# Performance work log

Measured on AMD Instinct MI355X. Metric: run time of the kernel, lower is better.

Reference implementation:

```python
import jax, jax.numpy as jnp
import numpy as np

B, L, E, H, T = 8, 4096, 512, 8, 2
D = E // H


def setup_inputs() -> dict:
    key = jax.random.key(0)
    ks = jax.random.split(key, 11)
    s = 0.02
    return {
        "query": jax.random.normal(ks[0], (B, L, E), jnp.float32),
        "key": jax.random.normal(ks[1], (B, L, E), jnp.float32),
        "value": jax.random.normal(ks[2], (B, L, E), jnp.float32),
        "Wq": jax.random.normal(ks[3], (T, E, E), jnp.float32) * s,
        "bq": jax.random.normal(ks[4], (T, E), jnp.float32) * s,
        "Wk": jax.random.normal(ks[5], (T, E, E), jnp.float32) * s,
        "bk": jax.random.normal(ks[6], (T, E), jnp.float32) * s,
        "Wv": jax.random.normal(ks[7], (E, E), jnp.float32) * s,
        "bv": jax.random.normal(ks[8], (E,), jnp.float32) * s,
        "Wout": jax.random.normal(ks[9], (E, E), jnp.float32) * s,
        "bout": jax.random.normal(ks[10], (E,), jnp.float32) * s,
    }


def reference(query, key, value, Wq, bq, Wk, bk, Wv, bv, Wout, bout):
    bsz, tgt_len, embed_dim = query.shape
    src_len = key.shape[1]
    n_head = H
    head_dim = embed_dim // n_head

    # value projection: (B,S,H,D)
    v = (value @ Wv.T + bv).reshape(bsz, src_len, n_head, head_dim)
    # faithful to torch: value.view(-1, bsz*n_head, head_dim).transpose(0,1)
    # WITHOUT permuting to (S,B,H,D) first -> pure memory reinterpretation
    v = jnp.swapaxes(v.reshape(src_len, bsz * n_head, head_dim), 0, 1)  # (BH,S,D)

    # per-term q/k projections -> (T,L,B,H,D) / (T,S,B,H,D)
    q = jnp.einsum('ble,tfe->tblf', query, Wq) + bq[:, None, None, :]
    k = jnp.einsum('bse,tfe->tbsf', key, Wk) + bk[:, None, None, :]
    q = q.reshape(T, bsz, tgt_len, n_head, head_dim).transpose(0, 2, 1, 3, 4)
    k = k.reshape(T, bsz, src_len, n_head, head_dim).transpose(0, 2, 1, 3, 4)

    # act_fun == softmax: q softmax over feature dim, k softmax over sequence dim (dim 0)
    q = jax.nn.softmax(q, axis=-1)
    k = jax.nn.softmax(k, axis=1)

    # flatten: (T, L, B*H, D) -> (T, B*H, L, D)
    q = jnp.swapaxes(q.reshape(T, tgt_len, bsz * n_head, head_dim), 1, 2)
    k = jnp.swapaxes(k.reshape(T, src_len, bsz * n_head, head_dim), 1, 2)

    # cosine positional reweighting (cosFormer): doubles feature dim
    m = max(src_len, tgt_len)
    idx = (np.pi / 2) * jnp.arange(1, m + 1, dtype=q.dtype) / m  # (m,)
    sin_q = jnp.sin(idx[:tgt_len])[None, None, :, None]
    cos_q = jnp.cos(idx[:tgt_len])[None, None, :, None]
    sin_k = jnp.sin(idx[:src_len])[None, None, :, None]
    cos_k = jnp.cos(idx[:src_len])[None, None, :, None]
    q = jnp.concatenate([q * sin_q, q * cos_q], axis=-1)  # (T,BH,L,2D)
    k = jnp.concatenate([k * sin_k, k * cos_k], axis=-1)  # (T,BH,S,2D)

    # linear attention: kv state then output, summed over terms
    kv = jnp.einsum('tnsd,nsm->tndm', k, v)          # (T,BH,2D,D)
    out = jnp.einsum('tnld,tndm->nlm', q, kv)        # (BH,L,D) summed over T

    # back to (B,L,E)
    out = jnp.swapaxes(out, 0, 1).reshape(tgt_len, bsz, embed_dim)
    out = jnp.swapaxes(out, 0, 1)
    return out @ Wout.T + bout
```

## Files before the change

### kernel.cpp

```cpp
#include <hip/hip_runtime.h>
#include <cstdio>

#define E_DIM 512
#define L_DIM 4096
#define B_DIM 8
#define H_DIM 8
#define T_DIM 2
#define M_ROWS 32768

typedef __attribute__((ext_vector_type(8))) __bf16 bf16x8;
typedef __attribute__((ext_vector_type(4))) float f32x4;

static __device__ __forceinline__ unsigned short f2bf(float f) {
  unsigned int u = __float_as_uint(f);
  return (unsigned short)((u + 0x7FFFu + ((u >> 16) & 1u)) >> 16);
}
static __device__ __forceinline__ unsigned int pkbf(float lo, float hi) {
  return (unsigned int)f2bf(lo) | ((unsigned int)f2bf(hi) << 16);
}
static __device__ __forceinline__ float bf2f(unsigned short u) {
  return __uint_as_float((unsigned int)u << 16);
}
static __device__ __forceinline__ void unpk8(uint4 u, float* f) {
  f[0] = bf2f((unsigned short)u.x); f[1] = bf2f((unsigned short)(u.x >> 16));
  f[2] = bf2f((unsigned short)u.y); f[3] = bf2f((unsigned short)(u.y >> 16));
  f[4] = bf2f((unsigned short)u.z); f[5] = bf2f((unsigned short)(u.z >> 16));
  f[6] = bf2f((unsigned short)u.w); f[7] = bf2f((unsigned short)(u.w >> 16));
}
static __device__ __forceinline__ int swz64(int row, int e) {
  return row * 64 + ((((e >> 3) ^ row) & 7) << 3) + (e & 7);
}
static __device__ __forceinline__ int swz128(int row, int e) {
  return row * 128 + ((((e >> 3) ^ row) & 7) << 3) + ((e >> 3) & 8) * 8 + (e & 7);
}
static __device__ __forceinline__ void gl_lds16(const unsigned short* g,
                                                unsigned short* l) {
  __builtin_amdgcn_global_load_lds(
      (const __attribute__((address_space(1))) unsigned int*)g,
      (__attribute__((address_space(3))) unsigned int*)l, 16, 0, 0);
}

__global__ void prep_kernel(const float* __restrict__ Wq, const float* __restrict__ Wk,
                            const float* __restrict__ Wv, const float* __restrict__ Wout,
                            unsigned short* __restrict__ wbf,
                            float* __restrict__ sintab, float* __restrict__ costab) {
  int blk = blockIdx.x;
  if (blk < 768) {
    int i8 = blk * 256 + threadIdx.x;
    const float* src;
    if (i8 < 65536) src = Wq + (size_t)i8 * 8;
    else if (i8 < 131072) src = Wk + (size_t)(i8 - 65536) * 8;
    else if (i8 < 163840) src = Wv + (size_t)(i8 - 131072) * 8;
    else src = Wout + (size_t)(i8 - 163840) * 8;
    float4 a = *(const float4*)src;
    float4 b = *(const float4*)(src + 4);
    uint4 o;
    o.x = pkbf(a.x, a.y); o.y = pkbf(a.z, a.w);
    o.z = pkbf(b.x, b.y); o.w = pkbf(b.z, b.w);
    *(uint4*)(wbf + (size_t)i8 * 8) = o;
  } else {
    int i = (blk - 768) * 256 + threadIdx.x;
    float idx = 1.57079632679489662f * (float)(i + 1) / (float)L_DIM;
    sintab[i] = sinf(idx);
    costab[i] = cosf(idx);
  }
}

__global__ void convf2b(const float* __restrict__ src, unsigned short* __restrict__ dst,
                        int n8) {
  for (int i = blockIdx.x * blockDim.x + threadIdx.x; i < n8; i += gridDim.x * blockDim.x) {
    float4 a = *(const float4*)(src + (size_t)i * 8);
    float4 b = *(const float4*)(src + (size_t)i * 8 + 4);
    uint4 o;
    o.x = pkbf(a.x, a.y); o.y = pkbf(a.z, a.w);
    o.z = pkbf(b.x, b.y); o.w = pkbf(b.z, b.w);
    *(uint4*)(dst + (size_t)i * 8) = o;
  }
}

#define YHALF 16777216
template <int MODE, int NBL2>
__global__ __launch_bounds__(256, 2) void gemm_xwt(
    const unsigned short* __restrict__ X, const unsigned short* __restrict__ W,
    const float* __restrict__ bias, void* __restrict__ Yv,
    float* __restrict__ psum) {
  __shared__ __align__(16) unsigned short smem[32768];
  __shared__ float sf2[256];
  const int tid = threadIdx.x;
  const int id = blockIdx.x;
  const int j = id >> 3;
  const int mb = (id & 7) * 32 + (j >> NBL2);
  const int nb = j & ((1 << NBL2) - 1);
  const int m0 = mb * 128, n0 = nb * 128;
  const int lane = tid & 63;
  const int w = tid >> 6;
  const int wr = w >> 1, wc = w & 1;
  const int lr = lane & 15;
  const int lk = (lane >> 4) * 8;
  const int rq = lane >> 4;
  const int srow = lane >> 3;
  const int gsrc8 = ((lane & 7) ^ srow) * 8;
  f32x4 acc[4][4];
#pragma unroll
  for (int i = 0; i < 4; ++i)
#pragma unroll
    for (int jj = 0; jj < 4; ++jj) acc[i][jj] = (f32x4){0.f, 0.f, 0.f, 0.f};

#pragma unroll
  for (int i = 0; i < 4; ++i) {
    int rb = w * 32 + i * 8;
    gl_lds16(X + (size_t)(m0 + rb + srow) * 512 + gsrc8, &smem[rb * 64]);
    gl_lds16(W + (size_t)(n0 + rb + srow) * 512 + gsrc8, &smem[8192 + rb * 64]);
  }
  __syncthreads();

#pragma unroll
  for (int step = 0; step < 8; ++step) {
    const int cur = step & 1;
    if (step < 7) {
      unsigned short* Ab = smem + (cur ^ 1) * 16384;
      const int kn = (step + 1) * 64;
#pragma unroll
      for (int i = 0; i < 4; ++i) {
        int rb = w * 32 + i * 8;
        gl_lds16(X + (size_t)(m0 + rb + srow) * 512 + kn + gsrc8, &Ab[rb * 64]);
        gl_lds16(W + (size_t)(n0 + rb + srow) * 512 + kn + gsrc8,
                 &Ab[8192 + rb * 64]);
      }
    }
    const unsigned short* As = smem + cur * 16384;
    const unsigned short* Bs = As + 8192;
#pragma unroll
    for (int kk = 0; kk < 2; ++kk) {
      bf16x8 av[4], bv[4];
      int ke = kk * 32 + lk;
#pragma unroll
      for (int fm = 0; fm < 4; ++fm)
        av[fm] = *(const bf16x8*)&As[swz64(wr * 64 + fm * 16 + lr, ke)];
#pragma unroll
      for (int fn = 0; fn < 4; ++fn)
        bv[fn] = *(const bf16x8*)&Bs[swz64(wc * 64 + fn * 16 + lr, ke)];
#pragma unroll
      for (int fm = 0; fm < 4; ++fm)
#pragma unroll
        for (int fn = 0; fn < 4; ++fn)
          acc[fm][fn] = __builtin_amdgcn_mfma_f32_16x16x32_bf16(av[fm], bv[fn],
                                                                acc[fm][fn], 0, 0, 0);
    }
    __syncthreads();
  }

  if (MODE == 0 || MODE == 2) {
    unsigned short* Cs = smem;
    if (MODE == 0) {
#pragma unroll
      for (int fn = 0; fn < 4; ++fn) {
        int col = wc * 64 + fn * 16 + lr;
        float bb = bias[n0 + col];
#pragma unroll
        for (int fm = 0; fm < 4; ++fm) {
          int row = wr * 64 + fm * 16 + rq * 4;
#pragma unroll
          for (int jj = 0; jj < 4; ++jj)
            Cs[(row + jj) * 136 + col] = f2bf(acc[fm][fn][jj] + bb);
        }
      }
    } else {
#pragma unroll
      for (int fn = 0; fn < 4; ++fn) {
        int col = wc * 64 + fn * 16 + lr;
        float bb = bias[n0 + col];
        float S = 0.f;
#pragma unroll
        for (int fm = 0; fm < 4; ++fm) {
          int row = wr * 64 + fm * 16 + rq * 4;
#pragma unroll
          for (int jj = 0; jj < 4; ++jj) {
            float u = __expf(acc[fm][fn][jj] + bb);
            S += u;
            Cs[(row + jj) * 136 + col] = f2bf(u);
          }
        }
        S += __shfl_xor(S, 16);
        S += __shfl_xor(S, 32);
        if (rq == 0) sf2[wr * 128 + col] = S;
      }
    }
    __syncthreads();
    if (MODE == 2 && tid < 128) {
      float S = sf2[tid] + sf2[128 + tid];
      psum[(size_t)(m0 >> 7) * (128 << NBL2) + n0 + tid] = S;
    }
    unsigned short* Yb = (unsigned short*)Yv + (size_t)(n0 >> 9) * YHALF;
    const int nc = n0 & 511;
#pragma unroll
    for (int i = 0; i < 8; ++i) {
      int idx = tid + i * 256;
      int row = idx >> 4, g = idx & 15;
      *(uint4*)(Yb + (size_t)(m0 + row) * 512 + nc + g * 8) =
          *(const uint4*)&Cs[row * 136 + g * 8];
    }
  } else {
    float* Cf = (float*)smem;
    float* Yf = (float*)Yv;
#pragma unroll
    for (int p = 0; p < 2; ++p) {
      if (p) __syncthreads();
      if (wr == p) {
#pragma unroll
        for (int fn = 0; fn < 4; ++fn) {
          int col = wc * 64 + fn * 16 + lr;
          float bb = bias[n0 + col];
#pragma unroll
          for (int fm = 0; fm < 4; ++fm) {
            int lrow = fm * 16 + rq * 4;
#pragma unroll
            for (int jj = 0; jj < 4; ++jj)
              Cf[(lrow + jj) * 132 + col] = acc[fm][fn][jj] + bb;
          }
        }
      }
      __syncthreads();
#pragma unroll
      for (int i = 0; i < 8; ++i) {
        int idx = tid + i * 256;
        int row = idx >> 5, g = idx & 31;
        *(float4*)(Yf + (size_t)(m0 + p * 64 + row) * 512 + n0 + g * 4) =
            *(const float4*)&Cf[row * 132 + g * 4];
      }
    }
  }
}

__global__ void colsum_reduce2(const float* __restrict__ psum,
                               float* __restrict__ colinv) {
  int t = blockIdx.x >> 4;
  int i = (blockIdx.x & 15) * 256 + threadIdx.x;
  int b = i >> 9, f = i & 511;
  float S = 0.f;
#pragma unroll
  for (int c = 0; c < 32; ++c)
    S += psum[(size_t)(b * 32 + c) * 1024 + t * 512 + f];
  colinv[t * 4096 + i] = 1.f / S;
}

__global__ __launch_bounds__(256) void kv_mfma(
    const unsigned short* __restrict__ Up, const unsigned short* __restrict__ Vpb,
    const float* __restrict__ sintab, const float* __restrict__ costab,
    float* __restrict__ kvpart) {
  __shared__ __align__(16) unsigned short kT[64 * 64];
  __shared__ __align__(16) unsigned short vT[128 * 64];
  const int tid = threadIdx.x;
  const int chunk = blockIdx.x;
  const int n = blockIdx.y;
  const int b = n >> 3, h = n & 7;
  const int lane = tid & 63;
  const int w = tid >> 6;
  const int lr = lane & 15;
  const int lk = (lane >> 4) * 8;
  const int sp = tid & 31;
  const int g = tid >> 5;
  f32x4 acc[4][2];
#pragma unroll
  for (int i = 0; i < 4; ++i) {
    acc[i][0] = (f32x4){0.f, 0.f, 0.f, 0.f};
    acc[i][1] = (f32x4){0.f, 0.f, 0.f, 0.f};
  }

  for (int st = 0; st < 8; ++st) {
    int sA = chunk * 512 + st * 64 + 2 * sp;
    const unsigned short* kp = Up + ((size_t)b * L_DIM + sA) * 512 + h * 64 + g * 8;
    uint4 ka = *(const uint4*)kp;
    uint4 kb = *(const uint4*)(kp + 512);
    int vr = ((sA >> 9) << 12) + ((sA & 511) << 3) + b;
    const unsigned short* vp = Vpb + (size_t)vr * 512 + h * 64 + g * 8;
    uint4 v0 = *(const uint4*)vp;
    uint4 v1 = *(const uint4*)(vp + 8 * 512);
    unsigned short ua[8], ub[8];
    *(uint4*)ua = ka;
    *(uint4*)ub = kb;
    float vA[8], vB[8];
    unpk8(v0, vA);
    unpk8(v1, vB);
    float sS = sintab[sA], sC = costab[sA];
    float tS = sintab[sA + 1], tC = costab[sA + 1];
    __syncthreads();
#pragma unroll
    for (int i = 0; i < 8; ++i) {
      int d = g * 8 + i;
      *(unsigned int*)&kT[swz64(d, 2 * sp)] =
          (unsigned int)ua[i] | ((unsigned int)ub[i] << 16);
    }
#pragma unroll
    for (int i = 0; i < 8; ++i) {
      int m = g * 8 + i;
      *(unsigned int*)&vT[swz64(m, 2 * sp)] = pkbf(vA[i] * sS, vB[i] * tS);
      *(unsigned int*)&vT[swz64(64 + m, 2 * sp)] = pkbf(vA[i] * sC, vB[i] * tC);
    }
    __syncthreads();
#pragma unroll
    for (int kk = 0; kk < 2; ++kk) {
      int ke = kk * 32 + lk;
      bf16x8 av[4], bv[2];
#pragma unroll
      for (int fm = 0; fm < 4; ++fm)
        av[fm] = *(const bf16x8*)&kT[swz64(fm * 16 + lr, ke)];
#pragma unroll
      for (int fn = 0; fn < 2; ++fn)
        bv[fn] = *(const bf16x8*)&vT[swz64(w * 32 + fn * 16 + lr, ke)];
#pragma unroll
      for (int fm = 0; fm < 4; ++fm)
#pragma unroll
        for (int fn = 0; fn < 2; ++fn)
          acc[fm][fn] = __builtin_amdgcn_mfma_f32_16x16x32_bf16(av[fm], bv[fn],
                                                                acc[fm][fn], 0, 0, 0);
    }
  }
  const int rq = lane >> 4;
#pragma unroll
  for (int fn = 0; fn < 2; ++fn) {
    int ncol = w * 32 + fn * 16 + lr;
    int m = ncol & 63;
    int ddbase = (ncol >> 6) * 64;
#pragma unroll
    for (int fm = 0; fm < 4; ++fm) {
#pragma unroll
      for (int jj = 0; jj < 4; ++jj) {
        int dd = ddbase + fm * 16 + rq * 4 + jj;
        kvpart[(((size_t)chunk * 64 + n) * 64 + m) * 128 + dd] = acc[fm][fn][jj];
      }
    }
  }
}

__global__ void kv_reduce_swz(const float* __restrict__ part,
                              const float* __restrict__ colinv,
                              unsigned short* __restrict__ kvT) {
  int i = blockIdx.x * 256 + threadIdx.x;
  float s = 0.f;
#pragma unroll
  for (int c = 0; c < 8; ++c) s += part[(size_t)c * 524288 + i];
  int dd = i & 127;
  int m = (i >> 7) & 63;
  int n = i >> 13;
  float sc = colinv[(n >> 3) * 512 + (n & 7) * 64 + (dd & 63)];
  int gg = dd >> 3;
  int e = ((gg & 8) | ((gg ^ m) & 7)) * 8 + (dd & 7);
  kvT[(size_t)(i >> 7) * 128 + e] = f2bf(s * sc);
}

__global__ __launch_bounds__(256) void out_fused(
    const unsigned short* __restrict__ Qp0, const unsigned short* __restrict__ Qp1,
    const unsigned short* __restrict__ kvT,
    const float* __restrict__ sintab, const float* __restrict__ costab,
    unsigned short* __restrict__ Yb) {
  __shared__ __align__(16) unsigned short q2s[64 * 128];
  __shared__ __align__(16) unsigned short kvs[2][64 * 128];
  const int tid = threadIdx.x;
  const int lc = blockIdx.x;
  const int n = blockIdx.y;
  const int b = n >> 3, h = n & 7;
  const int lane = tid & 63;
  const int w = tid >> 6;
  {
    const uint4* s0 = (const uint4*)(kvT + (size_t)n * 8192);
    const uint4* s1 = (const uint4*)(kvT + 524288 + (size_t)n * 8192);
    uint4* d0 = (uint4*)kvs[0];
    uint4* d1 = (uint4*)kvs[1];
#pragma unroll
    for (int i = 0; i < 4; ++i) {
      d0[tid + i * 256] = s0[tid + i * 256];
      d1[tid + i * 256] = s1[tid + i * 256];
    }
  }
  const int l0 = lc * 64;
  const int wr = w >> 1, wc = w & 1;
  const int lr = lane & 15;
  const int lk = (lane >> 4) * 8;
  const int rq = lane >> 4;
  f32x4 acc[2][2];
  acc[0][0] = acc[0][1] = acc[1][0] = acc[1][1] = (f32x4){0.f, 0.f, 0.f, 0.f};
#pragma unroll
  for (int t = 0; t < 2; ++t) {
    const unsigned short* Qp = t ? Qp1 : Qp0;
    if (t) __syncthreads();
#pragma unroll
    for (int i = 0; i < 2; ++i) {
      int idx = tid + i * 256;
      int row = idx >> 3;
      int g = idx & 7;
      uint4 q = *(const uint4*)(Qp + ((size_t)b * L_DIM + l0 + row) * 512 +
                                h * 64 + g * 8);
      float v[8];
      unpk8(q, v);
      float m8 = fmaxf(fmaxf(fmaxf(v[0], v[1]), fmaxf(v[2], v[3])),
                       fmaxf(fmaxf(v[4], v[5]), fmaxf(v[6], v[7])));
      m8 = fmaxf(m8, __shfl_xor(m8, 1));
      m8 = fmaxf(m8, __shfl_xor(m8, 2));
      m8 = fmaxf(m8, __shfl_xor(m8, 4));
      float e[8], s8;
#pragma unroll
      for (int k = 0; k < 8; ++k) e[k] = __expf(v[k] - m8);
      s8 = ((e[0] + e[1]) + (e[2] + e[3])) + ((e[4] + e[5]) + (e[6] + e[7]));
      s8 += __shfl_xor(s8, 1);
      s8 += __shfl_xor(s8, 2);
      s8 += __shfl_xor(s8, 4);
      float inv = 1.f / s8;
      int gl = l0 + row;
      float sn = sintab[gl] * inv;
      float cs = costab[gl] * inv;
      uint4 os, oc;
      os.x = pkbf(e[0] * sn, e[1] * sn); os.y = pkbf(e[2] * sn, e[3] * sn);
      os.z = pkbf(e[4] * sn, e[5] * sn); os.w = pkbf(e[6] * sn, e[7] * sn);
      oc.x = pkbf(e[0] * cs, e[1] * cs); oc.y = pkbf(e[2] * cs, e[3] * cs);
      oc.z = pkbf(e[4] * cs, e[5] * cs); oc.w = pkbf(e[6] * cs, e[7] * cs);
      *(uint4*)&q2s[swz128(row, g * 8)] = os;
      *(uint4*)&q2s[swz128(row, 64 + g * 8)] = oc;
    }
    __syncthreads();
#pragma unroll
    for (int ks = 0; ks < 4; ++ks) {
      int ke = ks * 32 + lk;
      bf16x8 av[2], bv[2];
#pragma unroll
      for (int fm = 0; fm < 2; ++fm)
        av[fm] = *(const bf16x8*)&q2s[swz128(wr * 32 + fm * 16 + lr, ke)];
#pragma unroll
      for (int fn = 0; fn < 2; ++fn)
        bv[fn] = *(const bf16x8*)&kvs[t][swz128(wc * 32 + fn * 16 + lr, ke)];
#pragma unroll
      for (int fm = 0; fm < 2; ++fm)
#pragma unroll
        for (int fn = 0; fn < 2; ++fn)
          acc[fm][fn] = __builtin_amdgcn_mfma_f32_16x16x32_bf16(av[fm], bv[fn],
                                                                acc[fm][fn], 0, 0, 0);
    }
  }
  __syncthreads();
  unsigned short* Os = q2s;
#pragma unroll
  for (int fn = 0; fn < 2; ++fn) {
    int col = wc * 32 + fn * 16 + lr;
#pragma unroll
    for (int fm = 0; fm < 2; ++fm) {
      int lrow = wr * 32 + fm * 16 + rq * 4;
#pragma unroll
      for (int jj = 0; jj < 4; ++jj)
        Os[(lrow + jj) * 72 + col] = f2bf(acc[fm][fn][jj]);
    }
  }
  __syncthreads();
#pragma unroll
  for (int i = 0; i < 2; ++i) {
    int idx = tid + i * 256;
    int row = idx >> 3, g = idx & 7;
    *(uint4*)(Yb + ((size_t)b * L_DIM + l0 + row) * 512 + h * 64 + g * 8) =
        *(const uint4*)&Os[row * 72 + g * 8];
  }
}

extern "C" void kernel_launch(void* const* d_in, const int* in_sizes, int n_in,
                              void* d_out, int out_size, void* d_ws, size_t ws_size,
                              hipStream_t stream) {
  const float* query = (const float*)d_in[0];
  const float* key   = (const float*)d_in[1];
  const float* value = (const float*)d_in[2];
  const float* Wq    = (const float*)d_in[3];
  const float* bq    = (const float*)d_in[4];
  const float* Wk    = (const float*)d_in[5];
  const float* bk    = (const float*)d_in[6];
  const float* Wv    = (const float*)d_in[7];
  const float* bv    = (const float*)d_in[8];
  const float* Wout  = (const float*)d_in[9];
  const float* bout  = (const float*)d_in[10];
  float* out = (float*)d_out;
  float* ws = (float*)d_ws;

  const size_t F_PROJ0 = 0;
  const size_t F_PROJ1 = F_PROJ0 + 8388608;
  const size_t F_VPB   = F_PROJ1 + 8388608;
  const size_t F_KVP   = F_VPB + 8388608;
  const size_t F_KVT   = F_KVP + 4194304;
  const size_t F_XBUF  = F_KVT + 524288;
  const size_t F_WBF   = F_XBUF + 8388608;
  const size_t F_CINV  = F_WBF + 786432;
  const size_t F_SIN   = F_CINV + 8192;
  const size_t F_COS   = F_SIN + 4096;
  const size_t TOTALF  = F_COS + 4096;
  if (ws_size < TOTALF * sizeof(float)) {
    fprintf(stderr, "kernel_launch: ws too small (%zu < %zu)\n", ws_size, TOTALF * 4);
    return;
  }
  unsigned short* proj0 = (unsigned short*)(ws + F_PROJ0);
  unsigned short* vpb   = (unsigned short*)(ws + F_VPB);
  float* kvpart = ws + F_KVP;
  unsigned short* kvT  = (unsigned short*)(ws + F_KVT);
  unsigned short* xbuf = (unsigned short*)(ws + F_XBUF);
  unsigned short* wbf  = (unsigned short*)(ws + F_WBF);
  float* cinv = ws + F_CINV;
  float* sintab = ws + F_SIN;
  float* costab = ws + F_COS;
  float* psum = kvpart;
  const size_t WQ_O = 0, WK_O = 524288, WV_O = 1048576, WOUT_O = 1310720;

  prep_kernel<<<784, 256, 0, stream>>>(Wq, Wk, Wv, Wout, wbf, sintab, costab);

  convf2b<<<2048, 256, 0, stream>>>(value, xbuf, 2097152);
  gemm_xwt<0, 2><<<1024, 256, 0, stream>>>(xbuf, wbf + WV_O, bv, vpb, nullptr);

  convf2b<<<2048, 256, 0, stream>>>(key, xbuf, 2097152);
  gemm_xwt<2, 3><<<2048, 256, 0, stream>>>(xbuf, wbf + WK_O, bk, proj0, psum);
  colsum_reduce2<<<32, 256, 0, stream>>>(psum, cinv);
  for (int t = 0; t < T_DIM; ++t) {
    unsigned short* projt = proj0 + (size_t)t * YHALF;
    kv_mfma<<<dim3(8, 64), 256, 0, stream>>>(projt, vpb, sintab, costab, kvpart);
    kv_reduce_swz<<<2048, 256, 0, stream>>>(kvpart, cinv + t * 4096,
                                            kvT + (size_t)t * 524288);
  }

  convf2b<<<2048, 256, 0, stream>>>(query, xbuf, 2097152);
  gemm_xwt<0, 3><<<2048, 256, 0, stream>>>(xbuf, wbf + WQ_O, bq, proj0, nullptr);
  out_fused<<<dim3(64, 64), 256, 0, stream>>>(proj0, proj0 + YHALF, kvT,
                                              sintab, costab, xbuf);
  gemm_xwt<1, 2><<<1024, 256, 0, stream>>>(xbuf, wbf + WOUT_O, bout, out, nullptr);
}
```

Measured before the change: 305.5 us.

## Use 256x256-tile 8-wave GEMM with staged prefetch for Q/K projections

Adds a new GEMM kernel with 256x256 output tiles, 512 threads, double-buffered LDS and prefetch of the next K-slice interleaved between MFMA phases with raised wave priority. It replaces the 128x128 kernel for the two wide (N=1024) Q and K projections, cutting how often X and W tiles are re-read and reducing block count. The K-projection partial column sums now come in 256-row chunks, so the reduction loop shrinks to 16 partials. It needs 128KB of LDS per block and a larger register footprint, which may limit occupancy.

```diff
diff --git a/kernel.cpp b/kernel.cpp
--- a/kernel.cpp
+++ b/kernel.cpp
@@ -79,13 +79,200 @@
 }
 
 #define YHALF 16777216
+
+template <int MODE>
+__global__ __launch_bounds__(512, 2) void gemm256(
+    const unsigned short* __restrict__ X, const unsigned short* __restrict__ W,
+    const float* __restrict__ bias, unsigned short* __restrict__ Yb0,
+    float* __restrict__ psum) {
+  __shared__ __align__(16) unsigned short smem[65536];
+  __shared__ float sf[2][256];
+  const int tid = threadIdx.x;
+  const int id = blockIdx.x;
+  const int j = id >> 3;
+  const int mb = (id & 7) * 16 + (j >> 2);
+  const int nb = j & 3;
+  const int m0 = mb * 256, n0 = nb * 256;
+  const int lane = tid & 63;
+  const int wid = tid >> 6;
+  const int wr = wid >> 2;
+  const int wc = wid & 3;
+  const int lr = lane & 15;
+  const int lk = (lane >> 4) * 8;
+  const int rq = lane >> 4;
+  const int wrow = wid * 8 + (lane >> 3);
+  const int gsrc8 = ((lane & 7) ^ (lane >> 3)) * 8;
+  const int wdst = wid * 512;
+
+  f32x4 acc[8][4];
+#pragma unroll
+  for (int i = 0; i < 8; ++i)
+#pragma unroll
+    for (int jj = 0; jj < 4; ++jj) acc[i][jj] = (f32x4){0.f, 0.f, 0.f, 0.f};
+
+  const unsigned short* Xm = X + (size_t)m0 * 512;
+  const unsigned short* Wn = W + (size_t)n0 * 512;
+
+#pragma unroll
+  for (int hh = 0; hh < 2; ++hh) {
+    gl_lds16(Xm + (size_t)(hh * 128 + wrow) * 512 + gsrc8,
+             smem + hh * 8192 + wdst);
+    gl_lds16(Xm + (size_t)(hh * 128 + 64 + wrow) * 512 + gsrc8,
+             smem + hh * 8192 + 4096 + wdst);
+    gl_lds16(Wn + (size_t)(hh * 128 + wrow) * 512 + gsrc8,
+             smem + 16384 + hh * 8192 + wdst);
+    gl_lds16(Wn + (size_t)(hh * 128 + 64 + wrow) * 512 + gsrc8,
+             smem + 16384 + hh * 8192 + 4096 + wdst);
+  }
+  asm volatile("s_waitcnt vmcnt(0)" ::: "memory");
+  __builtin_amdgcn_s_barrier();
+
+#pragma unroll
+  for (int kt = 0; kt < 8; ++kt) {
+    const int cur = (kt & 1) * 32768;
+    const int nxt = cur ^ 32768;
+    const int kn = (kt + 1) * 64;
+    const unsigned short* As = smem + cur + wr * 8192;
+    const unsigned short* Bs = smem + cur + 16384 + (wc >> 1) * 8192;
+    const int brow0 = (wc & 1) * 64;
+    bf16x8 av[4], bv[4];
+
+    if (kt < 7) {
+      gl_lds16(Xm + (size_t)wrow * 512 + kn + gsrc8, smem + nxt + wdst);
+      gl_lds16(Xm + (size_t)(64 + wrow) * 512 + kn + gsrc8,
+               smem + nxt + 4096 + wdst);
+    }
+#pragma unroll
+    for (int fn = 0; fn < 4; ++fn)
+      bv[fn] = *(const bf16x8*)&Bs[swz64(brow0 + fn * 16 + lr, lk)];
+#pragma unroll
+    for (int fm = 0; fm < 4; ++fm)
+      av[fm] = *(const bf16x8*)&As[swz64(fm * 16 + lr, lk)];
+    __builtin_amdgcn_s_setprio(1);
+#pragma unroll
+    for (int fm = 0; fm < 4; ++fm)
+#pragma unroll
+      for (int fn = 0; fn < 4; ++fn)
+        acc[fm][fn] = __builtin_amdgcn_mfma_f32_16x16x32_bf16(av[fm], bv[fn],
+                                                              acc[fm][fn], 0, 0, 0);
+    __builtin_amdgcn_s_setprio(0);
+    __builtin_amdgcn_s_barrier();
+
+    if (kt < 7) {
+      gl_lds16(Xm + (size_t)(128 + wrow) * 512 + kn + gsrc8,
+               smem + nxt + 8192 + wdst);
+      gl_lds16(Xm + (size_t)(192 + wrow) * 512 + kn + gsrc8,
+               smem + nxt + 8192 + 4096 + wdst);
+    }
+#pragma unroll
+    for (int fm = 0; fm < 4; ++fm)
+      av[fm] = *(const bf16x8*)&As[swz64((fm + 4) * 16 + lr, lk)];
+    __builtin_amdgcn_s_setprio(1);
+#pragma unroll
+    for (int fm = 0; fm < 4; ++fm)
+#pragma unroll
+      for (int fn = 0; fn < 4; ++fn)
+        acc[fm + 4][fn] = __builtin_amdgcn_mfma_f32_16x16x32_bf16(av[fm], bv[fn],
+                                                                  acc[fm + 4][fn], 0, 0, 0);
+    __builtin_amdgcn_s_setprio(0);
+    __builtin_amdgcn_s_barrier();
+
+    if (kt < 7) {
+      gl_lds16(Wn + (size_t)wrow * 512 + kn + gsrc8, smem + nxt + 16384 + wdst);
+      gl_lds16(Wn + (size_t)(64 + wrow) * 512 + kn + gsrc8,
+               smem + nxt + 16384 + 4096 + wdst);
+    }
+#pragma unroll
+    for (int fn = 0; fn < 4; ++fn)
+      bv[fn] = *(const bf16x8*)&Bs[swz64(brow0 + fn * 16 + lr, 32 + lk)];
+#pragma unroll
+    for (int fm = 0; fm < 4; ++fm)
+      av[fm] = *(const bf16x8*)&As[swz64(fm * 16 + lr, 32 + lk)];
+    __builtin_amdgcn_s_setprio(1);
+#pragma unroll
+    for (int fm = 0; fm < 4; ++fm)
+#pragma unroll
+      for (int fn = 0; fn < 4; ++fn)
+        acc[fm][fn] = __builtin_amdgcn_mfma_f32_16x16x32_bf16(av[fm], bv[fn],
+                                                              acc[fm][fn], 0, 0, 0);
+    __builtin_amdgcn_s_setprio(0);
+    __builtin_amdgcn_s_barrier();
+
+    if (kt < 7) {
+      gl_lds16(Wn + (size_t)(128 + wrow) * 512 + kn + gsrc8,
+               smem + nxt + 24576 + wdst);
+      gl_lds16(Wn + (size_t)(192 + wrow) * 512 + kn + gsrc8,
+               smem + nxt + 24576 + 4096 + wdst);
+    }
+#pragma unroll
+    for (int fm = 0; fm < 4; ++fm)
+      av[fm] = *(const bf16x8*)&As[swz64((fm + 4) * 16 + lr, 32 + lk)];
+    __builtin_amdgcn_s_setprio(1);
+#pragma unroll
+    for (int fm = 0; fm < 4; ++fm)
+#pragma unroll
+      for (int fn = 0; fn < 4; ++fn)
+        acc[fm + 4][fn] = __builtin_amdgcn_mfma_f32_16x16x32_bf16(av[fm], bv[fn],
+                                                                  acc[fm + 4][fn], 0, 0, 0);
+    __builtin_amdgcn_s_setprio(0);
+    asm volatile("s_waitcnt vmcnt(0)" ::: "memory");
+    __builtin_amdgcn_s_barrier();
+  }
+
+  unsigned short* Cs = smem;
+  unsigned short* Yb = Yb0 + (size_t)(n0 >> 9) * YHALF;
+  const int nc = n0 & 511;
+#pragma unroll
+  for (int p = 0; p < 2; ++p) {
+    __syncthreads();
+    if (wr == p) {
+#pragma unroll
+      for (int fn = 0; fn < 4; ++fn) {
+        int col = wc * 64 + fn * 16 + lr;
+        float bb = bias[n0 + col];
+        float S = 0.f;
+#pragma unroll
+        for (int fm = 0; fm < 8; ++fm) {
+          int row = fm * 16 + rq * 4;
+#pragma unroll
+          for (int jj = 0; jj < 4; ++jj) {
+            float v = acc[fm][fn][jj] + bb;
+            if (MODE == 2) {
+              v = __expf(v);
+              S += v;
+            }
+            Cs[(row + jj) * 264 + col] = f2bf(v);
+          }
+        }
+        if (MODE == 2) {
+          S += __shfl_xor(S, 16);
+          S += __shfl_xor(S, 32);
+          if (rq == 0) sf[p][col] = S;
+        }
+      }
+    }
+    __syncthreads();
+#pragma unroll
+    for (int i = 0; i < 8; ++i) {
+      int idx = tid + i * 512;
+      int row = idx >> 5, g = idx & 31;
+      *(uint4*)(Yb + (size_t)(m0 + p * 128 + row) * 512 + nc + g * 8) =
+          *(const uint4*)&Cs[row * 264 + g * 8];
+    }
+  }
+  if (MODE == 2) {
+    if (tid < 256) {
+      float S = sf[0][tid] + sf[1][tid];
+      psum[(size_t)(m0 >> 8) * 1024 + n0 + tid] = S;
+    }
+  }
+}
+
 template <int MODE, int NBL2>
 __global__ __launch_bounds__(256, 2) void gemm_xwt(
     const unsigned short* __restrict__ X, const unsigned short* __restrict__ W,
-    const float* __restrict__ bias, void* __restrict__ Yv,
-    float* __restrict__ psum) {
+    const float* __restrict__ bias, void* __restrict__ Yv) {
   __shared__ __align__(16) unsigned short smem[32768];
-  __shared__ float sf2[256];
   const int tid = threadIdx.x;
   const int id = blockIdx.x;
   const int j = id >> 3;
@@ -150,47 +337,21 @@
     __syncthreads();
   }
 
-  if (MODE == 0 || MODE == 2) {
+  if (MODE == 0) {
     unsigned short* Cs = smem;
-    if (MODE == 0) {
-#pragma unroll
-      for (int fn = 0; fn < 4; ++fn) {
-        int col = wc * 64 + fn * 16 + lr;
-        float bb = bias[n0 + col];
-#pragma unroll
-        for (int fm = 0; fm < 4; ++fm) {
-          int row = wr * 64 + fm * 16 + rq * 4;
-#pragma unroll
-          for (int jj = 0; jj < 4; ++jj)
-            Cs[(row + jj) * 136 + col] = f2bf(acc[fm][fn][jj] + bb);
-        }
+#pragma unroll
+    for (int fn = 0; fn < 4; ++fn) {
+      int col = wc * 64 + fn * 16 + lr;
+      float bb = bias[n0 + col];
+#pragma unroll
+      for (int fm = 0; fm < 4; ++fm) {
+        int row = wr * 64 + fm * 16 + rq * 4;
+#pragma unroll
+        for (int jj = 0; jj < 4; ++jj)
+          Cs[(row + jj) * 136 + col] = f2bf(acc[fm][fn][jj] + bb);
       }
-    } else {
-#pragma unroll
-      for (int fn = 0; fn < 4; ++fn) {
-        int col = wc * 64 + fn * 16 + lr;
-        float bb = bias[n0 + col];
-        float S = 0.f;
-#pragma unroll
-        for (int fm = 0; fm < 4; ++fm) {
-          int row = wr * 64 + fm * 16 + rq * 4;
-#pragma unroll
-          for (int jj = 0; jj < 4; ++jj) {
-            float u = __expf(acc[fm][fn][jj] + bb);
-            S += u;
-            Cs[(row + jj) * 136 + col] = f2bf(u);
-          }
-        }
-        S += __shfl_xor(S, 16);
-        S += __shfl_xor(S, 32);
-        if (rq == 0) sf2[wr * 128 + col] = S;
-      }
     }
     __syncthreads();
-    if (MODE == 2 && tid < 128) {
-      float S = sf2[tid] + sf2[128 + tid];
-      psum[(size_t)(m0 >> 7) * (128 << NBL2) + n0 + tid] = S;
-    }
     unsigned short* Yb = (unsigned short*)Yv + (size_t)(n0 >> 9) * YHALF;
     const int nc = n0 & 511;
 #pragma unroll
@@ -239,8 +400,8 @@
   int b = i >> 9, f = i & 511;
   float S = 0.f;
 #pragma unroll
-  for (int c = 0; c < 32; ++c)
-    S += psum[(size_t)(b * 32 + c) * 1024 + t * 512 + f];
+  for (int c = 0; c < 16; ++c)
+    S += psum[(size_t)(b * 16 + c) * 1024 + t * 512 + f];
   colinv[t * 4096 + i] = 1.f / S;
 }
 
@@ -506,10 +667,10 @@
   prep_kernel<<<784, 256, 0, stream>>>(Wq, Wk, Wv, Wout, wbf, sintab, costab);
 
   convf2b<<<2048, 256, 0, stream>>>(value, xbuf, 2097152);
-  gemm_xwt<0, 2><<<1024, 256, 0, stream>>>(xbuf, wbf + WV_O, bv, vpb, nullptr);
+  gemm_xwt<0, 2><<<1024, 256, 0, stream>>>(xbuf, wbf + WV_O, bv, vpb);
 
   convf2b<<<2048, 256, 0, stream>>>(key, xbuf, 2097152);
-  gemm_xwt<2, 3><<<2048, 256, 0, stream>>>(xbuf, wbf + WK_O, bk, proj0, psum);
+  gemm256<2><<<512, 512, 0, stream>>>(xbuf, wbf + WK_O, bk, proj0, psum);
   colsum_reduce2<<<32, 256, 0, stream>>>(psum, cinv);
   for (int t = 0; t < T_DIM; ++t) {
     unsigned short* projt = proj0 + (size_t)t * YHALF;
@@ -519,8 +680,8 @@
   }
 
   convf2b<<<2048, 256, 0, stream>>>(query, xbuf, 2097152);
-  gemm_xwt<0, 3><<<2048, 256, 0, stream>>>(xbuf, wbf + WQ_O, bq, proj0, nullptr);
+  gemm256<0><<<512, 512, 0, stream>>>(xbuf, wbf + WQ_O, bq, proj0, nullptr);
   out_fused<<<dim3(64, 64), 256, 0, stream>>>(proj0, proj0 + YHALF, kvT,
                                               sintab, costab, xbuf);
-  gemm_xwt<1, 2><<<1024, 256, 0, stream>>>(xbuf, wbf + WOUT_O, bout, out, nullptr);
-}
+  gemm_xwt<1, 2><<<1024, 256, 0, stream>>>(xbuf, wbf + WOUT_O, bout, out);
+}
```

After: 318.0 us. 1.04x slower.
